# Kernel optimization log

Measured on AMD Instinct MI355X. Metric: run time of the kernel, lower is better.

## Reference

```python
import jax, jax.numpy as jnp
import numpy as np

TEMPERATURE = 16.0  # sqrt(d_k) for d_k=256

def setup_inputs() -> dict:
    key = jax.random.key(0)
    q = jax.random.normal(key, (32, 1024, 256), dtype=jnp.float32)
    return {"q": q}

def reference(q):
    # attn = q @ q^T  (b, l, l)
    attn = jnp.einsum('bld,bmd->blm', q, q)
    # data-dependent zero mask -> -inf fill (before temperature scaling, matching torch order)
    zero_mask = attn == 0.0
    attn = jnp.where(zero_mask, -jnp.inf, attn / TEMPERATURE)
    attn = jax.nn.softmax(attn, axis=2)
    # rows that were fully -inf produce NaN -> zero them out
    attn = jnp.where(jnp.isnan(attn), 0.0, attn)
    # dropout is identity in eval/reference mode
    output = jnp.einsum('blm,bmd->bld', attn, q)
    return (output, attn)
```

## Files before the change

### kernel.cpp

```cpp
#include <hip/hip_runtime.h>
#include <stdint.h>

#define NB 32
#define NL 1024
#define ND 256
#define ROWU16 2048

typedef __attribute__((ext_vector_type(8))) __bf16 bf16x8;
typedef __attribute__((ext_vector_type(8))) uint16_t u16x8;
typedef __attribute__((ext_vector_type(4))) float f32x4;

__device__ __forceinline__ uint16_t f2bf(float f) {
  union { float f; uint32_t u; } v; v.f = f;
  return (uint16_t)((v.u + 0x7fffu + ((v.u >> 16) & 1u)) >> 16);
}
__device__ __forceinline__ float bf2f(uint16_t h) {
  union { uint32_t u; float f; } v; v.u = ((uint32_t)h) << 16;
  return v.f;
}

#define GLD_LDS16(g, l)                                                        \
  __builtin_amdgcn_global_load_lds(                                            \
      (__attribute__((address_space(1))) void*)(g),                            \
      (__attribute__((address_space(3))) void*)(l), 16, 0, 0)

__global__ __launch_bounds__(256) void convert_kernel(
    const float* __restrict__ q, uint16_t* __restrict__ qb,
    uint16_t* __restrict__ qt) {
  __shared__ uint16_t tile[64][72];
  int b = blockIdx.z;
  int l0 = blockIdx.x * 64, d0 = blockIdx.y * 64;
  int t = threadIdx.x;
  int r = t >> 4;
  int c4 = (t & 15) * 4;
  const float* qsrc = q + (size_t)b * NL * ND;
  uint16_t* qbb = qb + (size_t)b * NL * ND;
  uint16_t* qtb = qt + (size_t)b * ND * NL;
#pragma unroll
  for (int i = 0; i < 4; i++) {
    int row = r + 16 * i;
    float4 v = *(const float4*)(qsrc + (size_t)(l0 + row) * ND + d0 + c4);
    ushort4 h;
    h.x = f2bf(v.x); h.y = f2bf(v.y); h.z = f2bf(v.z); h.w = f2bf(v.w);
    *(ushort4*)(qbb + (size_t)(l0 + row) * ND + d0 + c4) = h;
    tile[row][c4 + 0] = h.x; tile[row][c4 + 1] = h.y;
    tile[row][c4 + 2] = h.z; tile[row][c4 + 3] = h.w;
  }
  __syncthreads();
#pragma unroll
  for (int i = 0; i < 4; i++) {
    int drow = r + 16 * i;
    ushort4 h;
    h.x = tile[c4 + 0][drow]; h.y = tile[c4 + 1][drow];
    h.z = tile[c4 + 2][drow]; h.w = tile[c4 + 3][drow];
    *(ushort4*)(qtb + (size_t)(d0 + drow) * NL + l0 + c4) = h;
  }
}

__global__ __launch_bounds__(256) void qk_kernel(
    const uint16_t* __restrict__ qb, float* __restrict__ attn_f32) {
  __shared__ alignas(16) uint16_t As[128 * 32];
  __shared__ alignas(16) uint16_t Bs[128 * 32];
  __shared__ float rp[128][2];
  int b = blockIdx.z;
  int m0 = blockIdx.x * 128, n0 = blockIdx.y * 128;
  const uint16_t* Q = qb + (size_t)b * NL * ND;
  int tid = threadIdx.x, lane = tid & 63, wave = tid >> 6;
  int wm = (wave & 1) * 64, wn = (wave >> 1) * 64;
  int quad = lane >> 4, l15 = lane & 15;
  f32x4 acc[4][4] = {};

  for (int k0 = 0; k0 < ND; k0 += 32) {
    __syncthreads();
#pragma unroll
    for (int i = 0; i < 2; i++) {
      int c = i * 256 + wave * 64 + lane;
      int row = c >> 2, cc = c & 3;
      int sw = (row >> 1) & 3;
      int gc = k0 + ((cc ^ sw) * 8);
      GLD_LDS16(Q + (size_t)(m0 + row) * ND + gc,
                As + (size_t)(i * 256 + wave * 64) * 8);
      GLD_LDS16(Q + (size_t)(n0 + row) * ND + gc,
                Bs + (size_t)(i * 256 + wave * 64) * 8);
    }
    __syncthreads();
    bf16x8 af[4], bfr[4];
#pragma unroll
    for (int t = 0; t < 4; t++) {
      int ra = wm + t * 16 + l15;
      af[t] = *(const bf16x8*)(As + ra * 32 + ((quad ^ ((ra >> 1) & 3)) * 8));
      int rb = wn + t * 16 + l15;
      bfr[t] = *(const bf16x8*)(Bs + rb * 32 + ((quad ^ ((rb >> 1) & 3)) * 8));
    }
#pragma unroll
    for (int tm = 0; tm < 4; tm++)
#pragma unroll
      for (int tn = 0; tn < 4; tn++)
        acc[tm][tn] = __builtin_amdgcn_mfma_f32_16x16x32_bf16(
            af[tm], bfr[tn], acc[tm][tn], 0, 0, 0);
  }

  const float kf = 0.09016844005555f;
  uint16_t* attn_u16 = (uint16_t*)attn_f32;
  size_t gbase = (size_t)b * NL;
#pragma unroll
  for (int tm = 0; tm < 4; tm++) {
    int rbl = wm + tm * 16 + quad * 4;
    float rsum[4] = {0.f, 0.f, 0.f, 0.f};
#pragma unroll
    for (int tn = 0; tn < 4; tn++) {
      int col = n0 + wn + tn * 16 + l15;
#pragma unroll
      for (int j = 0; j < 4; j++) {
        float s = acc[tm][tn][j];
        float e = (s == 0.0f) ? 0.0f : __builtin_amdgcn_exp2f(s * kf);
        attn_u16[(gbase + m0 + rbl + j) * ROWU16 + col] = f2bf(e);
        rsum[j] += e;
      }
    }
#pragma unroll
    for (int j = 0; j < 4; j++) {
      float v = rsum[j];
      v += __shfl_xor(v, 1, 64);
      v += __shfl_xor(v, 2, 64);
      v += __shfl_xor(v, 4, 64);
      v += __shfl_xor(v, 8, 64);
      if (l15 == 0) rp[rbl + j][wave >> 1] = v;
    }
  }
  __syncthreads();
  if (tid < 128) {
    float s = rp[tid][0] + rp[tid][1];
    attn_f32[(gbase + m0 + tid) * (size_t)NL + 512 + blockIdx.y] = s;
  }
}

__global__ __launch_bounds__(512) void pv_kernel(
    float* __restrict__ attn_f32, const uint16_t* __restrict__ qt,
    float* __restrict__ out) {
  __shared__ alignas(16) uint16_t As[128 * 32];
  __shared__ alignas(16) uint16_t Bs[256 * 32];
  __shared__ float inv_lds[128];
  int b = blockIdx.z;
  int m0 = blockIdx.x * 128;
  const uint16_t* Ap = (const uint16_t*)attn_f32 + (size_t)b * NL * ROWU16;
  const uint16_t* Bt = qt + (size_t)b * ND * NL;
  int tid = threadIdx.x, lane = tid & 63, wave = tid >> 6;
  int wm = (wave & 1) * 64, wn = (wave >> 1) * 64;
  int quad = lane >> 4, l15 = lane & 15;
  f32x4 acc[4][4] = {};

  if (tid < 128) {
    const float* pf = attn_f32 + (size_t)(b * NL + m0 + tid) * NL + 512;
    float s = pf[0] + pf[1] + pf[2] + pf[3] + pf[4] + pf[5] + pf[6] + pf[7];
    inv_lds[tid] = (s > 0.0f) ? 1.0f / s : 0.0f;
  }

  int xr = tid >> 2;
  int xc = tid & 3;
  int xsw = (xr >> 1) & 3;
  float* xdst_row = attn_f32 + (size_t)(b * NL + m0 + xr) * NL + xc * 8;

  for (int k0 = NL - 32; k0 >= 0; k0 -= 32) {
    __syncthreads();
    {
      int c = tid;
      int row = c >> 2, cc = c & 3;
      int sw = (row >> 1) & 3;
      int gc = k0 + ((cc ^ sw) * 8);
      GLD_LDS16(Ap + (size_t)(m0 + row) * ROWU16 + gc,
                As + (size_t)(wave * 64) * 8);
    }
#pragma unroll
    for (int i = 0; i < 2; i++) {
      int c = i * 512 + tid;
      int row = c >> 2, cc = c & 3;
      int sw = (row >> 1) & 3;
      int gc = k0 + ((cc ^ sw) * 8);
      GLD_LDS16(Bt + (size_t)row * NL + gc,
                Bs + (size_t)(i * 512 + wave * 64) * 8);
    }
    __syncthreads();
    bf16x8 af[4], bfr[4];
#pragma unroll
    for (int t = 0; t < 4; t++) {
      int ra = wm + t * 16 + l15;
      af[t] = *(const bf16x8*)(As + ra * 32 + ((quad ^ ((ra >> 1) & 3)) * 8));
      int rb = wn + t * 16 + l15;
      bfr[t] = *(const bf16x8*)(Bs + rb * 32 + ((quad ^ ((rb >> 1) & 3)) * 8));
    }
#pragma unroll
    for (int tm = 0; tm < 4; tm++)
#pragma unroll
      for (int tn = 0; tn < 4; tn++)
        acc[tm][tn] = __builtin_amdgcn_mfma_f32_16x16x32_bf16(
            af[tm], bfr[tn], acc[tm][tn], 0, 0, 0);

    {
      u16x8 hv = *(const u16x8*)(As + xr * 32 + ((xc ^ xsw) * 8));
      float inv = inv_lds[xr];
      float4 lo, hi;
      lo.x = bf2f(hv[0]) * inv;
      lo.y = bf2f(hv[1]) * inv;
      lo.z = bf2f(hv[2]) * inv;
      lo.w = bf2f(hv[3]) * inv;
      hi.x = bf2f(hv[4]) * inv;
      hi.y = bf2f(hv[5]) * inv;
      hi.z = bf2f(hv[6]) * inv;
      hi.w = bf2f(hv[7]) * inv;
      float4* dp = (float4*)(xdst_row + k0);
      dp[0] = lo;
      dp[1] = hi;
    }
  }

  float* O = out + (size_t)b * NL * ND;
#pragma unroll
  for (int tm = 0; tm < 4; tm++) {
    int rbl = wm + tm * 16 + quad * 4;
#pragma unroll
    for (int tn = 0; tn < 4; tn++) {
      int col = wn + tn * 16 + l15;
#pragma unroll
      for (int j = 0; j < 4; j++)
        O[(size_t)(m0 + rbl + j) * ND + col] = acc[tm][tn][j] * inv_lds[rbl + j];
    }
  }
}

extern "C" void kernel_launch(void* const* d_in, const int* in_sizes, int n_in,
                              void* d_out, int out_size, void* d_ws,
                              size_t ws_size, hipStream_t stream) {
  (void)in_sizes; (void)n_in; (void)out_size; (void)ws_size;
  const float* q = (const float*)d_in[0];
  float* out = (float*)d_out;
  float* attn = out + (size_t)NB * NL * ND;
  uint16_t* qb = (uint16_t*)d_ws;
  uint16_t* qt = qb + (size_t)NB * NL * ND;

  convert_kernel<<<dim3(16, 4, NB), 256, 0, stream>>>(q, qb, qt);
  qk_kernel<<<dim3(8, 8, NB), 256, 0, stream>>>(qb, attn);
  pv_kernel<<<dim3(8, 1, NB), 512, 0, stream>>>(attn, qt, out);
}
```

Measured before the change: 267.3 us.

## Halve PV row tile to 64 rows for more blocks, defer attn writeback

The PV kernel now handles 64 query rows per block with 256 threads, four waves that each split the 256 output columns, instead of 128 rows with 512 threads. This doubles the grid from 256 to 512 blocks to fill more CUs. The in-place fp32 attn writeback is held in registers and stored after the next barrier so it overlaps the following tile's loads. The QK kernel also uses the native bf16 cast instead of manual rounding. Each block still streams the full V^T, so global reads of qt double.

```diff
diff --git a/kernel.cpp b/kernel.cpp
--- a/kernel.cpp
+++ b/kernel.cpp
@@ -114,7 +114,9 @@
       for (int j = 0; j < 4; j++) {
         float s = acc[tm][tn][j];
         float e = (s == 0.0f) ? 0.0f : __builtin_amdgcn_exp2f(s * kf);
-        attn_u16[(gbase + m0 + rbl + j) * ROWU16 + col] = f2bf(e);
+        union { __bf16 b; uint16_t u; } cv;
+        cv.b = (__bf16)e;
+        attn_u16[(gbase + m0 + rbl + j) * ROWU16 + col] = cv.u;
         rsum[j] += e;
       }
     }
@@ -135,22 +137,22 @@
   }
 }
 
-__global__ __launch_bounds__(512) void pv_kernel(
+__global__ __launch_bounds__(256) void pv_kernel(
     float* __restrict__ attn_f32, const uint16_t* __restrict__ qt,
     float* __restrict__ out) {
-  __shared__ alignas(16) uint16_t As[128 * 32];
+  __shared__ alignas(16) uint16_t As[64 * 32];
   __shared__ alignas(16) uint16_t Bs[256 * 32];
-  __shared__ float inv_lds[128];
+  __shared__ float inv_lds[64];
   int b = blockIdx.z;
-  int m0 = blockIdx.x * 128;
+  int m0 = blockIdx.x * 64;
   const uint16_t* Ap = (const uint16_t*)attn_f32 + (size_t)b * NL * ROWU16;
   const uint16_t* Bt = qt + (size_t)b * ND * NL;
   int tid = threadIdx.x, lane = tid & 63, wave = tid >> 6;
-  int wm = (wave & 1) * 64, wn = (wave >> 1) * 64;
+  int wn = wave * 64;
   int quad = lane >> 4, l15 = lane & 15;
   f32x4 acc[4][4] = {};
 
-  if (tid < 128) {
+  if (tid < 64) {
     const float* pf = attn_f32 + (size_t)(b * NL + m0 + tid) * NL + 512;
     float s = pf[0] + pf[1] + pf[2] + pf[3] + pf[4] + pf[5] + pf[6] + pf[7];
     inv_lds[tid] = (s > 0.0f) ? 1.0f / s : 0.0f;
@@ -159,32 +161,38 @@
   int xr = tid >> 2;
   int xc = tid & 3;
   int xsw = (xr >> 1) & 3;
-  float* xdst_row = attn_f32 + (size_t)(b * NL + m0 + xr) * NL + xc * 8;
+  float* xrow = attn_f32 + (size_t)(b * NL + m0 + xr) * NL;
+
+  float4 p0, p1;
+  float* pdst = nullptr;
 
   for (int k0 = NL - 32; k0 >= 0; k0 -= 32) {
     __syncthreads();
+    if (k0 != NL - 32) {
+      ((float4*)pdst)[0] = p0;
+      ((float4*)pdst)[1] = p1;
+    }
     {
-      int c = tid;
-      int row = c >> 2, cc = c & 3;
+      int row = tid >> 2, cc = tid & 3;
       int sw = (row >> 1) & 3;
       int gc = k0 + ((cc ^ sw) * 8);
       GLD_LDS16(Ap + (size_t)(m0 + row) * ROWU16 + gc,
                 As + (size_t)(wave * 64) * 8);
     }
 #pragma unroll
-    for (int i = 0; i < 2; i++) {
-      int c = i * 512 + tid;
+    for (int i = 0; i < 4; i++) {
+      int c = i * 256 + tid;
       int row = c >> 2, cc = c & 3;
       int sw = (row >> 1) & 3;
       int gc = k0 + ((cc ^ sw) * 8);
       GLD_LDS16(Bt + (size_t)row * NL + gc,
-                Bs + (size_t)(i * 512 + wave * 64) * 8);
+                Bs + (size_t)(i * 256 + wave * 64) * 8);
     }
     __syncthreads();
     bf16x8 af[4], bfr[4];
 #pragma unroll
     for (int t = 0; t < 4; t++) {
-      int ra = wm + t * 16 + l15;
+      int ra = t * 16 + l15;
       af[t] = *(const bf16x8*)(As + ra * 32 + ((quad ^ ((ra >> 1) & 3)) * 8));
       int rb = wn + t * 16 + l15;
       bfr[t] = *(const bf16x8*)(Bs + rb * 32 + ((quad ^ ((rb >> 1) & 3)) * 8));
@@ -199,25 +207,24 @@
     {
       u16x8 hv = *(const u16x8*)(As + xr * 32 + ((xc ^ xsw) * 8));
       float inv = inv_lds[xr];
-      float4 lo, hi;
-      lo.x = bf2f(hv[0]) * inv;
-      lo.y = bf2f(hv[1]) * inv;
-      lo.z = bf2f(hv[2]) * inv;
-      lo.w = bf2f(hv[3]) * inv;
-      hi.x = bf2f(hv[4]) * inv;
-      hi.y = bf2f(hv[5]) * inv;
-      hi.z = bf2f(hv[6]) * inv;
-      hi.w = bf2f(hv[7]) * inv;
-      float4* dp = (float4*)(xdst_row + k0);
-      dp[0] = lo;
-      dp[1] = hi;
-    }
-  }
+      p0.x = bf2f(hv[0]) * inv;
+      p0.y = bf2f(hv[1]) * inv;
+      p0.z = bf2f(hv[2]) * inv;
+      p0.w = bf2f(hv[3]) * inv;
+      p1.x = bf2f(hv[4]) * inv;
+      p1.y = bf2f(hv[5]) * inv;
+      p1.z = bf2f(hv[6]) * inv;
+      p1.w = bf2f(hv[7]) * inv;
+      pdst = xrow + k0 + xc * 8;
+    }
+  }
+  ((float4*)pdst)[0] = p0;
+  ((float4*)pdst)[1] = p1;
 
   float* O = out + (size_t)b * NL * ND;
 #pragma unroll
   for (int tm = 0; tm < 4; tm++) {
-    int rbl = wm + tm * 16 + quad * 4;
+    int rbl = tm * 16 + quad * 4;
 #pragma unroll
     for (int tn = 0; tn < 4; tn++) {
       int col = wn + tn * 16 + l15;
@@ -240,5 +247,5 @@
 
   convert_kernel<<<dim3(16, 4, NB), 256, 0, stream>>>(q, qb, qt);
   qk_kernel<<<dim3(8, 8, NB), 256, 0, stream>>>(qb, attn);
-  pv_kernel<<<dim3(8, 1, NB), 512, 0, stream>>>(attn, qt, out);
-}
+  pv_kernel<<<dim3(16, 1, NB), 256, 0, stream>>>(attn, qt, out);
+}
```

New measurement: 266.4 us. Within noise of the previous version (-0.3%).

## Fuse QK, softmax and PV into one kernel with the probability tile kept in LDS

Applied to the files above, without the earlier changes.

Replaces the separate QK and PV kernels with a single kernel. Each block of 64 query rows computes a full 64x1024 row strip of exponentiated scores, stores it as bf16 in a swizzled 128KB LDS buffer, reduces row sums locally, then writes the normalized fp32 attention and runs the PV GEMM from LDS. This removes the bf16 round trip of attention through global memory and the scratch row-sum exchange. The cost is heavy LDS use, which allows only one block per CU, a grid of just 512 blocks, and recomputation of Q tiles for every block.

```diff
diff --git a/kernel.cpp b/kernel.cpp
--- a/kernel.cpp
+++ b/kernel.cpp
@@ -4,10 +4,9 @@
 #define NB 32
 #define NL 1024
 #define ND 256
-#define ROWU16 2048
 
 typedef __attribute__((ext_vector_type(8))) __bf16 bf16x8;
-typedef __attribute__((ext_vector_type(8))) uint16_t u16x8;
+typedef __attribute__((ext_vector_type(4))) uint16_t u16x4;
 typedef __attribute__((ext_vector_type(4))) float f32x4;
 
 __device__ __forceinline__ uint16_t f2bf(float f) {
@@ -57,173 +56,156 @@
   }
 }
 
-__global__ __launch_bounds__(256) void qk_kernel(
-    const uint16_t* __restrict__ qb, float* __restrict__ attn_f32) {
-  __shared__ alignas(16) uint16_t As[128 * 32];
-  __shared__ alignas(16) uint16_t Bs[128 * 32];
-  __shared__ float rp[128][2];
+__global__ __launch_bounds__(512) void attn_kernel(
+    const uint16_t* __restrict__ qb, const uint16_t* __restrict__ qt,
+    float* __restrict__ attn, float* __restrict__ out) {
+  __shared__ alignas(16) uint16_t P[64 * 1024];
+  __shared__ alignas(16) uint16_t pool[8192];
   int b = blockIdx.z;
-  int m0 = blockIdx.x * 128, n0 = blockIdx.y * 128;
+  int m0 = blockIdx.x * 64;
   const uint16_t* Q = qb + (size_t)b * NL * ND;
-  int tid = threadIdx.x, lane = tid & 63, wave = tid >> 6;
-  int wm = (wave & 1) * 64, wn = (wave >> 1) * 64;
-  int quad = lane >> 4, l15 = lane & 15;
-  f32x4 acc[4][4] = {};
-
-  for (int k0 = 0; k0 < ND; k0 += 32) {
-    __syncthreads();
-#pragma unroll
-    for (int i = 0; i < 2; i++) {
-      int c = i * 256 + wave * 64 + lane;
-      int row = c >> 2, cc = c & 3;
-      int sw = (row >> 1) & 3;
-      int gc = k0 + ((cc ^ sw) * 8);
-      GLD_LDS16(Q + (size_t)(m0 + row) * ND + gc,
-                As + (size_t)(i * 256 + wave * 64) * 8);
-      GLD_LDS16(Q + (size_t)(n0 + row) * ND + gc,
-                Bs + (size_t)(i * 256 + wave * 64) * 8);
-    }
-    __syncthreads();
-    bf16x8 af[4], bfr[4];
-#pragma unroll
-    for (int t = 0; t < 4; t++) {
-      int ra = wm + t * 16 + l15;
-      af[t] = *(const bf16x8*)(As + ra * 32 + ((quad ^ ((ra >> 1) & 3)) * 8));
-      int rb = wn + t * 16 + l15;
-      bfr[t] = *(const bf16x8*)(Bs + rb * 32 + ((quad ^ ((rb >> 1) & 3)) * 8));
-    }
-#pragma unroll
-    for (int tm = 0; tm < 4; tm++)
-#pragma unroll
-      for (int tn = 0; tn < 4; tn++)
-        acc[tm][tn] = __builtin_amdgcn_mfma_f32_16x16x32_bf16(
-            af[tm], bfr[tn], acc[tm][tn], 0, 0, 0);
-  }
-
-  const float kf = 0.09016844005555f;
-  uint16_t* attn_u16 = (uint16_t*)attn_f32;
-  size_t gbase = (size_t)b * NL;
-#pragma unroll
-  for (int tm = 0; tm < 4; tm++) {
-    int rbl = wm + tm * 16 + quad * 4;
-    float rsum[4] = {0.f, 0.f, 0.f, 0.f};
-#pragma unroll
-    for (int tn = 0; tn < 4; tn++) {
-      int col = n0 + wn + tn * 16 + l15;
-#pragma unroll
-      for (int j = 0; j < 4; j++) {
-        float s = acc[tm][tn][j];
-        float e = (s == 0.0f) ? 0.0f : __builtin_amdgcn_exp2f(s * kf);
-        attn_u16[(gbase + m0 + rbl + j) * ROWU16 + col] = f2bf(e);
-        rsum[j] += e;
-      }
-    }
-#pragma unroll
-    for (int j = 0; j < 4; j++) {
-      float v = rsum[j];
-      v += __shfl_xor(v, 1, 64);
-      v += __shfl_xor(v, 2, 64);
-      v += __shfl_xor(v, 4, 64);
-      v += __shfl_xor(v, 8, 64);
-      if (l15 == 0) rp[rbl + j][wave >> 1] = v;
-    }
-  }
-  __syncthreads();
-  if (tid < 128) {
-    float s = rp[tid][0] + rp[tid][1];
-    attn_f32[(gbase + m0 + tid) * (size_t)NL + 512 + blockIdx.y] = s;
-  }
-}
-
-__global__ __launch_bounds__(512) void pv_kernel(
-    float* __restrict__ attn_f32, const uint16_t* __restrict__ qt,
-    float* __restrict__ out) {
-  __shared__ alignas(16) uint16_t As[128 * 32];
-  __shared__ alignas(16) uint16_t Bs[256 * 32];
-  __shared__ float inv_lds[128];
-  int b = blockIdx.z;
-  int m0 = blockIdx.x * 128;
-  const uint16_t* Ap = (const uint16_t*)attn_f32 + (size_t)b * NL * ROWU16;
   const uint16_t* Bt = qt + (size_t)b * ND * NL;
   int tid = threadIdx.x, lane = tid & 63, wave = tid >> 6;
-  int wm = (wave & 1) * 64, wn = (wave >> 1) * 64;
+  int wmw = wave >> 1;
+  int wnh = wave & 1;
   int quad = lane >> 4, l15 = lane & 15;
-  f32x4 acc[4][4] = {};
-
-  if (tid < 128) {
-    const float* pf = attn_f32 + (size_t)(b * NL + m0 + tid) * NL + 512;
-    float s = pf[0] + pf[1] + pf[2] + pf[3] + pf[4] + pf[5] + pf[6] + pf[7];
-    inv_lds[tid] = (s > 0.0f) ? 1.0f / s : 0.0f;
-  }
-
-  int xr = tid >> 2;
-  int xc = tid & 3;
-  int xsw = (xr >> 1) & 3;
-  float* xdst_row = attn_f32 + (size_t)(b * NL + m0 + xr) * NL + xc * 8;
-
-  for (int k0 = NL - 32; k0 >= 0; k0 -= 32) {
-    __syncthreads();
-    {
-      int c = tid;
-      int row = c >> 2, cc = c & 3;
-      int sw = (row >> 1) & 3;
-      int gc = k0 + ((cc ^ sw) * 8);
-      GLD_LDS16(Ap + (size_t)(m0 + row) * ROWU16 + gc,
-                As + (size_t)(wave * 64) * 8);
-    }
+  int mw = wmw * 16 + l15;
+
+  bf16x8 af[8];
+#pragma unroll
+  for (int kk = 0; kk < 8; kk++)
+    af[kk] = *(const bf16x8*)(Q + (size_t)(m0 + mw) * ND + kk * 32 + quad * 8);
+
+  {
+    int row = tid >> 2, cc = tid & 3;
+    int sw = (row >> 1) & 3;
+    GLD_LDS16(Q + (size_t)row * ND + ((cc ^ sw) * 8),
+              pool + (size_t)(wave * 64) * 8);
+  }
+  float rsum[4] = {0.f, 0.f, 0.f, 0.f};
+  const float kf = 0.09016844005555f;
+  int buf = 0;
+  for (int ns = 0; ns < 8; ns++) {
+    f32x4 sacc[4] = {};
+    int n0 = ns * 128;
+#pragma unroll
+    for (int kk = 0; kk < 8; kk++) {
+      __syncthreads();
+      int step = ns * 8 + kk + 1;
+      if (step < 64) {
+        int nn0 = (step >> 3) * 128, kk0 = (step & 7) * 32;
+        int row = tid >> 2, cc = tid & 3;
+        int sw = (row >> 1) & 3;
+        GLD_LDS16(Q + (size_t)(nn0 + row) * ND + kk0 + ((cc ^ sw) * 8),
+                  pool + (size_t)((buf ^ 1) * 512 + wave * 64) * 8);
+      }
+      const uint16_t* Bb = pool + buf * 4096;
+      bf16x8 bq[4];
+#pragma unroll
+      for (int t = 0; t < 4; t++) {
+        int rb = wnh * 64 + t * 16 + l15;
+        bq[t] = *(const bf16x8*)(Bb + rb * 32 + ((quad ^ ((rb >> 1) & 3)) * 8));
+      }
+#pragma unroll
+      for (int t = 0; t < 4; t++)
+        sacc[t] = __builtin_amdgcn_mfma_f32_16x16x32_bf16(af[kk], bq[t],
+                                                          sacc[t], 0, 0, 0);
+      buf ^= 1;
+    }
+#pragma unroll
+    for (int t = 0; t < 4; t++) {
+      int n = n0 + wnh * 64 + t * 16 + l15;
+      int g = n >> 3, e = n & 7;
+#pragma unroll
+      for (int j = 0; j < 4; j++) {
+        int m = wmw * 16 + quad * 4 + j;
+        float s = sacc[t][j];
+        float ev = (s == 0.0f) ? 0.0f : __builtin_amdgcn_exp2f(s * kf);
+        P[m * 1024 + (((g ^ (m & 7)) << 3) + e)] = f2bf(ev);
+        rsum[j] += ev;
+      }
+    }
+  }
+
+  __syncthreads();
+  float* poolf = (float*)pool;
+#pragma unroll
+  for (int j = 0; j < 4; j++) {
+    float v = rsum[j];
+    v += __shfl_xor(v, 1, 64);
+    v += __shfl_xor(v, 2, 64);
+    v += __shfl_xor(v, 4, 64);
+    v += __shfl_xor(v, 8, 64);
+    if (l15 == 0) poolf[(wmw * 16 + quad * 4 + j) * 2 + wnh] = v;
+  }
+  __syncthreads();
+  float invo[4];
+#pragma unroll
+  for (int j = 0; j < 4; j++) {
+    int r = wmw * 16 + quad * 4 + j;
+    float s = poolf[r * 2] + poolf[r * 2 + 1];
+    invo[j] = (s > 0.f) ? 1.f / s : 0.f;
+  }
+  int xm = tid >> 3, xs = tid & 7;
+  float sx = poolf[xm * 2] + poolf[xm * 2 + 1];
+  float invx = (sx > 0.f) ? 1.f / sx : 0.f;
+  __syncthreads();
+
+  f32x4 pacc[8] = {};
+  {
 #pragma unroll
     for (int i = 0; i < 2; i++) {
       int c = i * 512 + tid;
       int row = c >> 2, cc = c & 3;
       int sw = (row >> 1) & 3;
-      int gc = k0 + ((cc ^ sw) * 8);
-      GLD_LDS16(Bt + (size_t)row * NL + gc,
-                Bs + (size_t)(i * 512 + wave * 64) * 8);
-    }
+      GLD_LDS16(Bt + (size_t)row * NL + ((cc ^ sw) * 8),
+                pool + (size_t)(i * 512 + wave * 64) * 8);
+    }
+  }
+  float* attnb = attn + ((size_t)b * NL + m0) * NL;
+  for (int c = 0; c < 32; c++) {
     __syncthreads();
-    bf16x8 af[4], bfr[4];
-#pragma unroll
-    for (int t = 0; t < 4; t++) {
-      int ra = wm + t * 16 + l15;
-      af[t] = *(const bf16x8*)(As + ra * 32 + ((quad ^ ((ra >> 1) & 3)) * 8));
-      int rb = wn + t * 16 + l15;
-      bfr[t] = *(const bf16x8*)(Bs + rb * 32 + ((quad ^ ((rb >> 1) & 3)) * 8));
-    }
-#pragma unroll
-    for (int tm = 0; tm < 4; tm++)
-#pragma unroll
-      for (int tn = 0; tn < 4; tn++)
-        acc[tm][tn] = __builtin_amdgcn_mfma_f32_16x16x32_bf16(
-            af[tm], bfr[tn], acc[tm][tn], 0, 0, 0);
-
-    {
-      u16x8 hv = *(const u16x8*)(As + xr * 32 + ((xc ^ xsw) * 8));
-      float inv = inv_lds[xr];
-      float4 lo, hi;
-      lo.x = bf2f(hv[0]) * inv;
-      lo.y = bf2f(hv[1]) * inv;
-      lo.z = bf2f(hv[2]) * inv;
-      lo.w = bf2f(hv[3]) * inv;
-      hi.x = bf2f(hv[4]) * inv;
-      hi.y = bf2f(hv[5]) * inv;
-      hi.z = bf2f(hv[6]) * inv;
-      hi.w = bf2f(hv[7]) * inv;
-      float4* dp = (float4*)(xdst_row + k0);
-      dp[0] = lo;
-      dp[1] = hi;
-    }
-  }
-
-  float* O = out + (size_t)b * NL * ND;
-#pragma unroll
-  for (int tm = 0; tm < 4; tm++) {
-    int rbl = wm + tm * 16 + quad * 4;
-#pragma unroll
-    for (int tn = 0; tn < 4; tn++) {
-      int col = wn + tn * 16 + l15;
-#pragma unroll
-      for (int j = 0; j < 4; j++)
-        O[(size_t)(m0 + rbl + j) * ND + col] = acc[tm][tn][j] * inv_lds[rbl + j];
+    int gx = c * 4 + (xs >> 1);
+    u16x4 h =
+        *(const u16x4*)(P + xm * 1024 + (((gx ^ (xm & 7)) << 3) + (xs & 1) * 4));
+    float4 v4;
+    v4.x = bf2f(h[0]) * invx; v4.y = bf2f(h[1]) * invx;
+    v4.z = bf2f(h[2]) * invx; v4.w = bf2f(h[3]) * invx;
+    *(float4*)(attnb + (size_t)xm * NL + c * 32 + xs * 4) = v4;
+    int gP = c * 4 + quad;
+    bf16x8 pa = *(const bf16x8*)(P + mw * 1024 + ((gP ^ (mw & 7)) << 3));
+    bf16x8 vb[8];
+#pragma unroll
+    for (int t = 0; t < 8; t++) {
+      int rb = wnh * 128 + t * 16 + l15;
+      vb[t] = *(const bf16x8*)(pool + rb * 32 + ((quad ^ ((rb >> 1) & 3)) * 8));
+    }
+    __syncthreads();
+    if (c < 31) {
+      int n0c = (c + 1) * 32;
+#pragma unroll
+      for (int i = 0; i < 2; i++) {
+        int cc2 = i * 512 + tid;
+        int row = cc2 >> 2, ccc = cc2 & 3;
+        int sw = (row >> 1) & 3;
+        GLD_LDS16(Bt + (size_t)row * NL + n0c + ((ccc ^ sw) * 8),
+                  pool + (size_t)(i * 512 + wave * 64) * 8);
+      }
+    }
+#pragma unroll
+    for (int t = 0; t < 8; t++)
+      pacc[t] = __builtin_amdgcn_mfma_f32_16x16x32_bf16(pa, vb[t], pacc[t],
+                                                        0, 0, 0);
+  }
+
+  float* O = out + (size_t)b * NL * ND + (size_t)m0 * ND;
+#pragma unroll
+  for (int t = 0; t < 8; t++) {
+    int col = wnh * 128 + t * 16 + l15;
+#pragma unroll
+    for (int j = 0; j < 4; j++) {
+      int r = wmw * 16 + quad * 4 + j;
+      O[(size_t)r * ND + col] = pacc[t][j] * invo[j];
     }
   }
 }
@@ -239,6 +221,5 @@
   uint16_t* qt = qb + (size_t)NB * NL * ND;
 
   convert_kernel<<<dim3(16, 4, NB), 256, 0, stream>>>(q, qb, qt);
-  qk_kernel<<<dim3(8, 8, NB), 256, 0, stream>>>(qb, attn);
-  pv_kernel<<<dim3(8, 1, NB), 512, 0, stream>>>(attn, qt, out);
-}
+  attn_kernel<<<dim3(16, 1, NB), 512, 0, stream>>>(qb, qt, attn, out);
+}
```

Measured after the change: 263.0 us. About the same (-1.6%).
